# Kernel optimization log

Hardware: AMD Instinct MI355X
Metric: run time of the kernel (lower is better)

## Reference

```python
import jax, jax.numpy as jnp
import numpy as np

B, T, NQ, NK = 2, 8, 128, 128
DIM_IN, DIM_OUT = 64, 256


def setup_inputs() -> dict:
    key = jax.random.key(0)
    ks = jax.random.split(key, 6)
    scale = 0.05  # keep tanh out of full saturation
    return {
        "query": jax.random.normal(ks[0], (B, NQ, DIM_IN), dtype=jnp.float32),
        "keys": jax.random.normal(ks[1], (B, T, NK, DIM_IN), dtype=jnp.float32),
        "Wq": jax.random.normal(ks[2], (DIM_IN, DIM_OUT), dtype=jnp.float32) * scale,
        "Wk": jax.random.normal(ks[3], (DIM_IN, DIM_OUT), dtype=jnp.float32) * scale,
        "bk": jax.random.normal(ks[4], (DIM_OUT,), dtype=jnp.float32) * scale,
        "v": jax.random.normal(ks[5], (DIM_OUT,), dtype=jnp.float32) * scale,
    }


def reference(query, keys, Wq, Wk, bk, v):
    # q: [B, Nq, D], k: [B, T, Nk, D]
    q = jnp.einsum("bqi,id->bqd", query, Wq)
    k = jnp.einsum("btki,id->btkd", keys, Wk) + bk
    # broadcast add -> [B, T, Nq, Nk, D], tanh, then score projection D->1
    h = jnp.tanh(q[:, None, :, None, :] + k[:, :, None, :, :])
    scores = jnp.einsum("btqkd,d->btqk", h, v)
    return jax.nn.softmax(scores, axis=-1)
```

## Files before the change

### kernel.cpp

```cpp
#include <hip/hip_runtime.h>

#define C_TANH 2.8853900817779268f
#define LOG2E  1.4426950408889634f

__device__ __forceinline__ float tanh_exact(float x) {
  float e = __builtin_amdgcn_exp2f(C_TANH * x);
  return 1.0f - 2.0f * __builtin_amdgcn_rcpf(1.0f + e);
}

__global__ __launch_bounds__(256) void proj_kernel(
    const float* __restrict__ query, const float* __restrict__ keys,
    const float* __restrict__ Wq, const float* __restrict__ Wk,
    const float* __restrict__ bk, float* __restrict__ q1t,
    float* __restrict__ k2t) {
  int bid = blockIdx.x;
  int d   = threadIdx.x;
  if (bid < 256) {
    int bt = bid >> 4;
    int kg = bid & 15;
    __shared__ float4 krows4[128];
    if (threadIdx.x < 128)
      krows4[threadIdx.x] =
          ((const float4*)(keys + bt * 8192 + kg * 512))[threadIdx.x];
    __syncthreads();
    float acc[8];
    float bias = bk[d];
#pragma unroll
    for (int kk = 0; kk < 8; ++kk) acc[kk] = bias;
#pragma unroll 4
    for (int i4 = 0; i4 < 16; ++i4) {
      float wa = Wk[(i4 * 4 + 0) * 256 + d];
      float wb = Wk[(i4 * 4 + 1) * 256 + d];
      float wc = Wk[(i4 * 4 + 2) * 256 + d];
      float wd = Wk[(i4 * 4 + 3) * 256 + d];
#pragma unroll
      for (int kk = 0; kk < 8; ++kk) {
        float4 kr = krows4[kk * 16 + i4];
        acc[kk] = fmaf(kr.x, wa, acc[kk]);
        acc[kk] = fmaf(kr.y, wb, acc[kk]);
        acc[kk] = fmaf(kr.z, wc, acc[kk]);
        acc[kk] = fmaf(kr.w, wd, acc[kk]);
      }
    }
#pragma unroll
    for (int kk = 0; kk < 8; ++kk)
      k2t[(bt * 256 + d) * 128 + kg * 8 + kk] = tanh_exact(acc[kk]);
  } else {
    int row = bid - 256;
    __shared__ float qrow[64];
    if (threadIdx.x < 64) qrow[threadIdx.x] = query[row * 64 + threadIdx.x];
    __syncthreads();
    float acc = 0.f;
#pragma unroll
    for (int i = 0; i < 64; ++i) acc += qrow[i] * Wq[i * 256 + d];
    q1t[row * 256 + d] = tanh_exact(acc);
  }
}

__global__ __launch_bounds__(256, 4) void score_kernel(
    const float* __restrict__ q1t, const float* __restrict__ v,
    const float* __restrict__ k2t, float* __restrict__ out) {
  __shared__ float  tb[64 * 128];
  __shared__ float2 qv[4 * 256];
  int tid = threadIdx.x;
  int wid = tid >> 6;
  int kk  = tid & 63;
  int blk = blockIdx.x;
  int bt  = blk >> 5;
  int qg  = blk & 31;
  int b   = bt >> 3;
  int q0  = qg * 4;

  for (int i = tid; i < 1024; i += 256) {
    int rr = i >> 8;
    int d  = i & 255;
    qv[i] = make_float2(q1t[(b * 128 + q0 + rr) * 256 + d], v[d] * LOG2E);
  }

  const float* ksrc = k2t + bt * 32768;
  float2 acc = make_float2(0.f, 0.f);

#pragma unroll
  for (int h = 0; h < 4; ++h) {
    __syncthreads();
    const float4* src4 = (const float4*)(ksrc + h * 8192);
    float4* dst4 = (float4*)tb;
    for (int i = tid; i < 2048; i += 256) dst4[i] = src4[i];
    __syncthreads();

    const float2* tb2 = (const float2*)tb;
#pragma unroll 8
    for (int d = 0; d < 64; ++d) {
      float2 tav = qv[wid * 256 + h * 64 + d];
      float2 tbv = tb2[d * 64 + kk];
      float n0 = tav.x + tbv.x;
      float n1 = tav.x + tbv.y;
      float d0 = fmaf(tav.x, tbv.x, 1.0f);
      float d1 = fmaf(tav.x, tbv.y, 1.0f);
      float r0 = n0 * __builtin_amdgcn_rcpf(d0);
      float r1 = n1 * __builtin_amdgcn_rcpf(d1);
      acc.x = fmaf(tav.y, r0, acc.x);
      acc.y = fmaf(tav.y, r1, acc.y);
    }
  }

  float s0 = acc.x, s1 = acc.y;
  float m = fmaxf(s0, s1);
#pragma unroll
  for (int off = 32; off > 0; off >>= 1) m = fmaxf(m, __shfl_xor(m, off, 64));
  float e0 = __builtin_amdgcn_exp2f(s0 - m);
  float e1 = __builtin_amdgcn_exp2f(s1 - m);
  float ssum = e0 + e1;
#pragma unroll
  for (int off = 32; off > 0; off >>= 1) ssum += __shfl_xor(ssum, off, 64);
  float inv = __builtin_amdgcn_rcpf(ssum);

  int row = bt * 128 + q0 + wid;
  ((float2*)(out + row * 128))[kk] = make_float2(e0 * inv, e1 * inv);
}

extern "C" void kernel_launch(void* const* d_in, const int* in_sizes, int n_in,
                              void* d_out, int out_size, void* d_ws, size_t ws_size,
                              hipStream_t stream) {
  const float* query = (const float*)d_in[0];
  const float* keys  = (const float*)d_in[1];
  const float* Wq    = (const float*)d_in[2];
  const float* Wk    = (const float*)d_in[3];
  const float* bk    = (const float*)d_in[4];
  const float* v     = (const float*)d_in[5];
  float* out = (float*)d_out;

  float* ws  = (float*)d_ws;
  float* q1t = ws;
  float* k2t = ws + 65536;

  proj_kernel<<<512, 256, 0, stream>>>(query, keys, Wq, Wk, bk, q1t, k2t);
  score_kernel<<<512, 256, 0, stream>>>(q1t, v, k2t, out);
}
```

Before: 88.61 us.

## Fuse projection and score kernels via cooperative grid sync

Merges the projection and scoring kernels into one cooperative kernel that shares a single shared-memory buffer and separates the phases with a grid-wide barrier. This removes the second kernel launch and the gap between launches. In exchange it adds a grid sync cost, requires all 512 blocks to be co-resident, and caps occupancy with a launch bound of 2 blocks per SM.

Measured after the change: 211.0 us. 138% more time.

```diff
diff --git a/kernel.cpp b/kernel.cpp
--- a/kernel.cpp
+++ b/kernel.cpp
@@ -1,4 +1,7 @@
 #include <hip/hip_runtime.h>
+#include <hip/hip_cooperative_groups.h>
+
+namespace cg = cooperative_groups;
 
 #define C_TANH 2.8853900817779268f
 #define LOG2E  1.4426950408889634f
@@ -8,21 +11,25 @@
   return 1.0f - 2.0f * __builtin_amdgcn_rcpf(1.0f + e);
 }
 
-__global__ __launch_bounds__(256) void proj_kernel(
+__global__ __launch_bounds__(256, 2) void fused_kernel(
     const float* __restrict__ query, const float* __restrict__ keys,
     const float* __restrict__ Wq, const float* __restrict__ Wk,
-    const float* __restrict__ bk, float* __restrict__ q1t,
-    float* __restrict__ k2t) {
+    const float* __restrict__ bk, const float* __restrict__ v,
+    float* __restrict__ q1t, float* __restrict__ k2t,
+    float* __restrict__ out) {
+  __shared__ __align__(16) float smem[64 * 128 + 2 * 1024];
+
+  int tid = threadIdx.x;
   int bid = blockIdx.x;
-  int d   = threadIdx.x;
+
   if (bid < 256) {
+    float4* krows4 = (float4*)smem;
     int bt = bid >> 4;
     int kg = bid & 15;
-    __shared__ float4 krows4[128];
-    if (threadIdx.x < 128)
-      krows4[threadIdx.x] =
-          ((const float4*)(keys + bt * 8192 + kg * 512))[threadIdx.x];
+    if (tid < 128)
+      krows4[tid] = ((const float4*)(keys + bt * 8192 + kg * 512))[tid];
     __syncthreads();
+    int d = tid;
     float acc[8];
     float bias = bk[d];
 #pragma unroll
@@ -46,28 +53,28 @@
     for (int kk = 0; kk < 8; ++kk)
       k2t[(bt * 256 + d) * 128 + kg * 8 + kk] = tanh_exact(acc[kk]);
   } else {
+    float* qrow = smem;
     int row = bid - 256;
-    __shared__ float qrow[64];
-    if (threadIdx.x < 64) qrow[threadIdx.x] = query[row * 64 + threadIdx.x];
+    if (tid < 64) qrow[tid] = query[row * 64 + tid];
     __syncthreads();
+    int d = tid;
     float acc = 0.f;
 #pragma unroll
     for (int i = 0; i < 64; ++i) acc += qrow[i] * Wq[i * 256 + d];
     q1t[row * 256 + d] = tanh_exact(acc);
   }
-}
 
-__global__ __launch_bounds__(256, 4) void score_kernel(
-    const float* __restrict__ q1t, const float* __restrict__ v,
-    const float* __restrict__ k2t, float* __restrict__ out) {
-  __shared__ float  tb[64 * 128];
-  __shared__ float2 qv[4 * 256];
-  int tid = threadIdx.x;
+  __syncthreads();
+  __threadfence();
+  cg::this_grid().sync();
+
+  float*  tb = smem;
+  float2* qv = (float2*)(smem + 64 * 128);
+
   int wid = tid >> 6;
   int kk  = tid & 63;
-  int blk = blockIdx.x;
-  int bt  = blk >> 5;
-  int qg  = blk & 31;
+  int bt  = bid >> 5;
+  int qg  = bid & 31;
   int b   = bt >> 3;
   int q0  = qg * 4;
 
@@ -134,6 +141,7 @@
   float* q1t = ws;
   float* k2t = ws + 65536;
 
-  proj_kernel<<<512, 256, 0, stream>>>(query, keys, Wq, Wk, bk, q1t, k2t);
-  score_kernel<<<512, 256, 0, stream>>>(q1t, v, k2t, out);
+  void* args[] = {&query, &keys, &Wq, &Wk, &bk, &v, &q1t, &k2t, &out};
+  hipLaunchCooperativeKernel((void*)fused_kernel, dim3(512), dim3(256), args,
+                             0, stream);
 }
```
